# Kernel optimization log

Hardware: AMD Instinct MI355X
Metric: run time of the kernel (lower is better)

The kernel has to match this reference:

```python
import jax, jax.numpy as jnp
import numpy as np

NUM_EMBEDDINGS = 512
EMBEDDING_DIM = 64
COMMITMENT_COST = 0.25


def setup_inputs() -> dict:
    key = jax.random.key(0)
    k1, k2 = jax.random.split(key)
    x = jax.random.normal(k1, (32, 64, 64, 64), dtype=jnp.float32)  # [B, C=D, H, W]
    # torch init: uniform(-1/K, 1/K)
    w = jax.random.uniform(k2, (NUM_EMBEDDINGS, EMBEDDING_DIM), dtype=jnp.float32,
                           minval=-1.0 / NUM_EMBEDDINGS, maxval=1.0 / NUM_EMBEDDINGS)
    return {"x": x, "w": w}


def reference(x, w):
    # [B, C, H, W] -> [B, H, W, C]
    xt = jnp.transpose(x, (0, 2, 3, 1))
    flat = xt.reshape(-1, EMBEDDING_DIM)  # [N, D]
    # squared L2 distances to each codebook vector: [N, K]
    distances = (jnp.sum(flat * flat, axis=1, keepdims=True)
                 + jnp.sum(w * w, axis=1)
                 - 2.0 * flat @ w.T)
    idx = jnp.argmin(distances, axis=1)  # [N]
    encodings = jax.nn.one_hot(idx, NUM_EMBEDDINGS, dtype=x.dtype)  # [N, K]
    quantized = w[idx].reshape(xt.shape)  # gather == one_hot @ w
    e_latent_loss = jnp.mean((jax.lax.stop_gradient(quantized) - xt) ** 2)
    q_latent_loss = jnp.mean((quantized - jax.lax.stop_gradient(xt)) ** 2)
    quant_loss = q_latent_loss + COMMITMENT_COST * e_latent_loss
    # straight-through estimator
    quantized_st = xt + jax.lax.stop_gradient(quantized - xt)
    quantized_out = jnp.transpose(quantized_st, (0, 3, 1, 2))  # back to [B, C, H, W]
    avg_probs = jnp.mean(encodings, axis=0)
    perplexity = jnp.exp(-jnp.sum(avg_probs * jnp.log(avg_probs + 1e-10)))
    return quantized_out, quant_loss, encodings, perplexity
```

## Files before the change

### kernel.cpp

```cpp
#include <hip/hip_runtime.h>
#include <math.h>

#define TB        256
#define POSB      64
#define GROUPS    4
#define KPG       128
#define NPOS      131072
#define KCODES    512
#define DIM       64
#define HW        4096
#define LOSS_OFF  8388608ull
#define ENC_OFF   8388609ull
#define PERP_OFF  75497473ull

__device__ __forceinline__ float tree8(float r0, float r1, float r2, float r3,
                                       float r4, float r5, float r6, float r7) {
    return __fadd_rn(__fadd_rn(__fadd_rn(r0, r1), __fadd_rn(r2, r3)),
                     __fadd_rn(__fadd_rn(r4, r5), __fadd_rn(r6, r7)));
}

extern "C" __global__ __launch_bounds__(512)
void vq_prep(const float* __restrict__ w, float* __restrict__ ww,
             int* __restrict__ counts, float* __restrict__ lossAcc)
{
    const int k = threadIdx.x;
    const float* wk = w + k * DIM;
    float r[8];
    #pragma unroll
    for (int i = 0; i < 8; ++i) {
        #pragma unroll
        for (int j = 0; j < 8; ++j) {
            float v = wk[i * 8 + j];
            float pp = __fmul_rn(v, v);
            r[j] = (i == 0) ? pp : __fadd_rn(r[j], pp);
        }
    }
    ww[k] = tree8(r[0], r[1], r[2], r[3], r[4], r[5], r[6], r[7]);
    counts[k] = 0;
    if (k == 0) *lossAcc = 0.0f;
}

extern "C" __global__ __launch_bounds__(TB)
__attribute__((amdgpu_waves_per_eu(2, 4)))
void vq_main(const float* __restrict__ x, const float* __restrict__ w,
             const float* __restrict__ ww, float* __restrict__ out,
             int* __restrict__ counts, float* __restrict__ lossAcc)
{
    __shared__ float cdist[GROUPS][POSB];
    __shared__ int   ckidx[GROUPS][POSB];
    __shared__ int   hcount[KCODES];

    const int tid = threadIdx.x;
    const int l   = tid & 63;
    const int g   = __builtin_amdgcn_readfirstlane(tid >> 6);
    const int n   = blockIdx.x * POSB + l;
    const int b   = n >> 12;
    const int hw  = n & 4095;

    hcount[tid]      = 0;
    hcount[tid + TB] = 0;

    const float* xp = x + ((size_t)b * DIM) * HW + hw;
    float x2[DIM];
    float r[8];
    #pragma unroll
    for (int i = 0; i < 8; ++i) {
        #pragma unroll
        for (int j = 0; j < 8; ++j) {
            const int d = i * 8 + j;
            float v = xp[(size_t)d * HW];
            x2[d] = v + v;
            float pp = __fmul_rn(v, v);
            r[j] = (i == 0) ? pp : __fadd_rn(r[j], pp);
        }
    }
    const float A = tree8(r[0], r[1], r[2], r[3], r[4], r[5], r[6], r[7]);

    float best  = INFINITY;
    int   bestk = 0;
    const size_t T0 = ENC_OFF + (size_t)blockIdx.x * (POSB * KCODES);
    float4* zs4 = reinterpret_cast<float4*>(out + T0 + 3);
    const float4 zero4 = make_float4(0.0f, 0.0f, 0.0f, 0.0f);

    for (int kk = 0; kk < KPG; ++kk) {
        const int k = g * KPG + kk;
        const float* wk = w + (size_t)k * DIM;
        float s[8];
        #pragma unroll
        for (int i = 0; i < 8; ++i) {
            #pragma unroll
            for (int j = 0; j < 8; ++j) {
                const int d = i * 8 + j;
                if (i == 0) s[j] = __fmul_rn(x2[d], wk[d]);
                else        s[j] = __fmaf_rn(x2[d], wk[d], s[j]);
            }
        }
        float dot  = tree8(s[0], s[1], s[2], s[3], s[4], s[5], s[6], s[7]);
        float t    = __fadd_rn(A, ww[k]);
        float dist = __fadd_rn(t, -dot);
        if (dist < best) { best = dist; bestk = k; }

        if ((kk & 3) == 0) {
            const int m = (kk >> 2) * TB + tid;
            if (m < 8191) zs4[m] = zero4;
        }
    }
    cdist[g][l] = best;
    ckidx[g][l] = bestk;

    if (tid < 3)  out[T0 + tid]   = 0.0f;
    if (tid == 3) out[T0 + 32767] = 0.0f;

    __syncthreads();

    float fb = cdist[0][l];
    int   fk = ckidx[0][l];
    #pragma unroll
    for (int gg = 1; gg < GROUPS; ++gg) {
        float dg = cdist[gg][l];
        int   kg = ckidx[gg][l];
        if (dg < fb) { fb = dg; fk = kg; }
    }

    if (g == 0) {
        out[ENC_OFF + (size_t)n * KCODES + fk] = 1.0f;
        atomicAdd(&hcount[fk], 1);

        const float4* wrow = reinterpret_cast<const float4*>(w + (size_t)fk * DIM);
        float* qo = out + ((size_t)b * DIM) * HW + hw;
        float sse = 0.0f;
        #pragma unroll
        for (int c = 0; c < 16; ++c) {
            float4 q = wrow[c];
            qo[(size_t)(4 * c + 0) * HW] = q.x;
            qo[(size_t)(4 * c + 1) * HW] = q.y;
            qo[(size_t)(4 * c + 2) * HW] = q.z;
            qo[(size_t)(4 * c + 3) * HW] = q.w;
            float e0 = q.x - 0.5f * x2[4 * c + 0]; sse = __fmaf_rn(e0, e0, sse);
            float e1 = q.y - 0.5f * x2[4 * c + 1]; sse = __fmaf_rn(e1, e1, sse);
            float e2 = q.z - 0.5f * x2[4 * c + 2]; sse = __fmaf_rn(e2, e2, sse);
            float e3 = q.w - 0.5f * x2[4 * c + 3]; sse = __fmaf_rn(e3, e3, sse);
        }
        #pragma unroll
        for (int off = 32; off > 0; off >>= 1) sse += __shfl_down(sse, off);
        if (l == 0) atomicAdd(lossAcc, sse);
    }

    __syncthreads();

    {
        int c0 = hcount[tid];       if (c0) atomicAdd(&counts[tid], c0);
        int c1 = hcount[tid + TB];  if (c1) atomicAdd(&counts[tid + TB], c1);
    }
}

extern "C" __global__ __launch_bounds__(512)
void vq_finalize(const int* __restrict__ counts, const float* __restrict__ lossAcc,
                 float* __restrict__ out)
{
    __shared__ double sred[KCODES];
    const int t = threadIdx.x;
    double p = (double)counts[t] * (1.0 / (double)NPOS);
    sred[t] = -p * log(p + 1e-10);
    __syncthreads();
    for (int s = KCODES / 2; s > 0; s >>= 1) {
        if (t < s) sred[t] += sred[t + s];
        __syncthreads();
    }
    if (t == 0) {
        out[PERP_OFF] = (float)exp(sred[0]);
        out[LOSS_OFF] = 1.25f * (lossAcc[0] / 8388608.0f);
    }
}

extern "C" void kernel_launch(void* const* d_in, const int* in_sizes, int n_in,
                              void* d_out, int out_size, void* d_ws, size_t ws_size,
                              hipStream_t stream)
{
    const float* x = (const float*)d_in[0];
    const float* w = (const float*)d_in[1];
    float* out = (float*)d_out;

    float* ww      = (float*)d_ws;
    int*   counts  = (int*)((char*)d_ws + 2048);
    float* lossAcc = (float*)((char*)d_ws + 4096);

    vq_prep<<<1, 512, 0, stream>>>(w, ww, counts, lossAcc);
    vq_main<<<NPOS / POSB, TB, 0, stream>>>(x, w, ww, out, counts, lossAcc);
    vq_finalize<<<1, 512, 0, stream>>>(counts, lossAcc, out);
}
```

Measured before the change: 450.2 us.

## Split one-hot zero fill into separate kernel and raise scan occupancy

Moves zeroing of the 256 MB one-hot encodings buffer out of the distance-scan loop into a dedicated streaming fill kernel launched before the scan. The scan kernel gets a higher waves-per-EU hint (4-8) and stores the doubled input as float4 registers. Fill order versus the scan's one-hot writes stays correct because both kernels run in order on the same stream. The intent is to let the write-bound fill and the compute-bound scan each run at their own best occupancy. The cost is an extra launch, and the fill no longer hides behind the FMA work.

```diff
diff --git a/kernel.cpp b/kernel.cpp
--- a/kernel.cpp
+++ b/kernel.cpp
@@ -12,6 +12,7 @@
 #define LOSS_OFF  8388608ull
 #define ENC_OFF   8388609ull
 #define PERP_OFF  75497473ull
+#define ENC_LEN   67108864ull
 
 __device__ __forceinline__ float tree8(float r0, float r1, float r2, float r3,
                                        float r4, float r5, float r6, float r7) {
@@ -40,9 +41,27 @@
     if (k == 0) *lossAcc = 0.0f;
 }
 
+extern "C" __global__ __launch_bounds__(256)
+void vq_fill(float* __restrict__ out)
+{
+    const float4 zero4 = make_float4(0.0f, 0.0f, 0.0f, 0.0f);
+    float4* dst = reinterpret_cast<float4*>(out + ENC_OFF + 3);
+    const size_t base = (size_t)blockIdx.x * (256 * 8) + threadIdx.x;
+    #pragma unroll
+    for (int i = 0; i < 8; ++i) {
+        const size_t m = base + (size_t)i * 256;
+        if (m < 16777215ull) dst[m] = zero4;
+    }
+    if (blockIdx.x == 0 && threadIdx.x < 4) {
+        const size_t d = (threadIdx.x < 3) ? (ENC_OFF + threadIdx.x)
+                                           : (ENC_OFF + ENC_LEN - 1);
+        out[d] = 0.0f;
+    }
+}
+
 extern "C" __global__ __launch_bounds__(TB)
-__attribute__((amdgpu_waves_per_eu(2, 4)))
-void vq_main(const float* __restrict__ x, const float* __restrict__ w,
+__attribute__((amdgpu_waves_per_eu(4, 8)))
+void vq_scan(const float* __restrict__ x, const float* __restrict__ w,
              const float* __restrict__ ww, float* __restrict__ out,
              int* __restrict__ counts, float* __restrict__ lossAcc)
 {
@@ -61,55 +80,54 @@
     hcount[tid + TB] = 0;
 
     const float* xp = x + ((size_t)b * DIM) * HW + hw;
-    float x2[DIM];
+    float4 x2[16];
     float r[8];
     #pragma unroll
-    for (int i = 0; i < 8; ++i) {
-        #pragma unroll
-        for (int j = 0; j < 8; ++j) {
-            const int d = i * 8 + j;
-            float v = xp[(size_t)d * HW];
-            x2[d] = v + v;
-            float pp = __fmul_rn(v, v);
-            r[j] = (i == 0) ? pp : __fadd_rn(r[j], pp);
-        }
+    for (int c = 0; c < 16; ++c) {
+        float v0 = xp[(size_t)(4 * c + 0) * HW];
+        float v1 = xp[(size_t)(4 * c + 1) * HW];
+        float v2 = xp[(size_t)(4 * c + 2) * HW];
+        float v3 = xp[(size_t)(4 * c + 3) * HW];
+        x2[c].x = v0 + v0; x2[c].y = v1 + v1;
+        x2[c].z = v2 + v2; x2[c].w = v3 + v3;
+        const int j = (c & 1) * 4;
+        float p0 = __fmul_rn(v0, v0), p1 = __fmul_rn(v1, v1);
+        float p2 = __fmul_rn(v2, v2), p3 = __fmul_rn(v3, v3);
+        if (c < 2) { r[j] = p0; r[j+1] = p1; r[j+2] = p2; r[j+3] = p3; }
+        else { r[j]   = __fadd_rn(r[j],   p0); r[j+1] = __fadd_rn(r[j+1], p1);
+               r[j+2] = __fadd_rn(r[j+2], p2); r[j+3] = __fadd_rn(r[j+3], p3); }
     }
     const float A = tree8(r[0], r[1], r[2], r[3], r[4], r[5], r[6], r[7]);
 
     float best  = INFINITY;
     int   bestk = 0;
-    const size_t T0 = ENC_OFF + (size_t)blockIdx.x * (POSB * KCODES);
-    float4* zs4 = reinterpret_cast<float4*>(out + T0 + 3);
-    const float4 zero4 = make_float4(0.0f, 0.0f, 0.0f, 0.0f);
-
     for (int kk = 0; kk < KPG; ++kk) {
         const int k = g * KPG + kk;
         const float* wk = w + (size_t)k * DIM;
         float s[8];
         #pragma unroll
-        for (int i = 0; i < 8; ++i) {
-            #pragma unroll
-            for (int j = 0; j < 8; ++j) {
-                const int d = i * 8 + j;
-                if (i == 0) s[j] = __fmul_rn(x2[d], wk[d]);
-                else        s[j] = __fmaf_rn(x2[d], wk[d], s[j]);
+        for (int c = 0; c < 16; ++c) {
+            const int j = (c & 1) * 4;
+            const float* wc = wk + 4 * c;
+            if (c < 2) {
+                s[j]   = __fmul_rn(x2[c].x, wc[0]);
+                s[j+1] = __fmul_rn(x2[c].y, wc[1]);
+                s[j+2] = __fmul_rn(x2[c].z, wc[2]);
+                s[j+3] = __fmul_rn(x2[c].w, wc[3]);
+            } else {
+                s[j]   = __fmaf_rn(x2[c].x, wc[0], s[j]);
+                s[j+1] = __fmaf_rn(x2[c].y, wc[1], s[j+1]);
+                s[j+2] = __fmaf_rn(x2[c].z, wc[2], s[j+2]);
+                s[j+3] = __fmaf_rn(x2[c].w, wc[3], s[j+3]);
             }
         }
         float dot  = tree8(s[0], s[1], s[2], s[3], s[4], s[5], s[6], s[7]);
         float t    = __fadd_rn(A, ww[k]);
         float dist = __fadd_rn(t, -dot);
         if (dist < best) { best = dist; bestk = k; }
-
-        if ((kk & 3) == 0) {
-            const int m = (kk >> 2) * TB + tid;
-            if (m < 8191) zs4[m] = zero4;
-        }
     }
     cdist[g][l] = best;
     ckidx[g][l] = bestk;
-
-    if (tid < 3)  out[T0 + tid]   = 0.0f;
-    if (tid == 3) out[T0 + 32767] = 0.0f;
 
     __syncthreads();
 
@@ -136,10 +154,10 @@
             qo[(size_t)(4 * c + 1) * HW] = q.y;
             qo[(size_t)(4 * c + 2) * HW] = q.z;
             qo[(size_t)(4 * c + 3) * HW] = q.w;
-            float e0 = q.x - 0.5f * x2[4 * c + 0]; sse = __fmaf_rn(e0, e0, sse);
-            float e1 = q.y - 0.5f * x2[4 * c + 1]; sse = __fmaf_rn(e1, e1, sse);
-            float e2 = q.z - 0.5f * x2[4 * c + 2]; sse = __fmaf_rn(e2, e2, sse);
-            float e3 = q.w - 0.5f * x2[4 * c + 3]; sse = __fmaf_rn(e3, e3, sse);
+            float e0 = q.x - 0.5f * x2[c].x; sse = __fmaf_rn(e0, e0, sse);
+            float e1 = q.y - 0.5f * x2[c].y; sse = __fmaf_rn(e1, e1, sse);
+            float e2 = q.z - 0.5f * x2[c].z; sse = __fmaf_rn(e2, e2, sse);
+            float e3 = q.w - 0.5f * x2[c].w; sse = __fmaf_rn(e3, e3, sse);
         }
         #pragma unroll
         for (int off = 32; off > 0; off >>= 1) sse += __shfl_down(sse, off);
@@ -186,6 +204,7 @@
     float* lossAcc = (float*)((char*)d_ws + 4096);
 
     vq_prep<<<1, 512, 0, stream>>>(w, ww, counts, lossAcc);
-    vq_main<<<NPOS / POSB, TB, 0, stream>>>(x, w, ww, out, counts, lossAcc);
+    vq_fill<<<8192, 256, 0, stream>>>(out);
+    vq_scan<<<NPOS / POSB, TB, 0, stream>>>(x, w, ww, out, counts, lossAcc);
     vq_finalize<<<1, 512, 0, stream>>>(counts, lossAcc, out);
 }
```

New measurement: 523.5 us. +16.3%, slower.

## Stage x rows in LDS, cooperatively load, and process two codes per iteration

Applied to the files above, without the earlier changes.

Each of the four waves now loads a quarter of the 64 channels for the block's positions into a padded LDS array, so x is read from global memory once per block instead of once per wave. The distance loop reads x from LDS and evaluates two codebook rows per iteration, giving two independent FMA chains and sharing each LDS load between them. The waves_per_eu hint is removed, and the encoding-zeroing stores are reissued on the new two-code schedule. In exchange, every FMA now needs an LDS read where it used a register before, which may limit the inner loop, and the added LDS use may lower occupancy.

```diff
diff --git a/kernel.cpp b/kernel.cpp
--- a/kernel.cpp
+++ b/kernel.cpp
@@ -5,10 +5,12 @@
 #define POSB      64
 #define GROUPS    4
 #define KPG       128
+#define KB        2
 #define NPOS      131072
 #define KCODES    512
 #define DIM       64
 #define HW        4096
+#define STRIDE    65
 #define LOSS_OFF  8388608ull
 #define ENC_OFF   8388609ull
 #define PERP_OFF  75497473ull
@@ -41,11 +43,11 @@
 }
 
 extern "C" __global__ __launch_bounds__(TB)
-__attribute__((amdgpu_waves_per_eu(2, 4)))
-void vq_main(const float* __restrict__ x, const float* __restrict__ w,
+void vq_scan(const float* __restrict__ x, const float* __restrict__ w,
              const float* __restrict__ ww, float* __restrict__ out,
              int* __restrict__ counts, float* __restrict__ lossAcc)
 {
+    __shared__ float x2ls[POSB * STRIDE];
     __shared__ float cdist[GROUPS][POSB];
     __shared__ int   ckidx[GROUPS][POSB];
     __shared__ int   hcount[KCODES];
@@ -61,16 +63,22 @@
     hcount[tid + TB] = 0;
 
     const float* xp = x + ((size_t)b * DIM) * HW + hw;
-    float x2[DIM];
+    float* row = &x2ls[l * STRIDE];
+    #pragma unroll
+    for (int t = 0; t < 16; ++t) {
+        const int d = 16 * g + t;
+        float v = xp[(size_t)d * HW];
+        row[d] = v + v;
+    }
+    __syncthreads();
+
     float r[8];
     #pragma unroll
     for (int i = 0; i < 8; ++i) {
         #pragma unroll
         for (int j = 0; j < 8; ++j) {
-            const int d = i * 8 + j;
-            float v = xp[(size_t)d * HW];
-            x2[d] = v + v;
-            float pp = __fmul_rn(v, v);
+            float xe = 0.5f * row[i * 8 + j];
+            float pp = __fmul_rn(xe, xe);
             r[j] = (i == 0) ? pp : __fadd_rn(r[j], pp);
         }
     }
@@ -82,26 +90,40 @@
     float4* zs4 = reinterpret_cast<float4*>(out + T0 + 3);
     const float4 zero4 = make_float4(0.0f, 0.0f, 0.0f, 0.0f);
 
-    for (int kk = 0; kk < KPG; ++kk) {
-        const int k = g * KPG + kk;
-        const float* wk = w + (size_t)k * DIM;
-        float s[8];
-        #pragma unroll
-        for (int i = 0; i < 8; ++i) {
-            #pragma unroll
-            for (int j = 0; j < 8; ++j) {
-                const int d = i * 8 + j;
-                if (i == 0) s[j] = __fmul_rn(x2[d], wk[d]);
-                else        s[j] = __fmaf_rn(x2[d], wk[d], s[j]);
+    for (int p = 0; p < KPG / KB; ++p) {
+        const int k0 = g * KPG + p * KB;
+        const float* w0 = w + (size_t)k0 * DIM;
+        float s0[8], s1[8];
+        #pragma unroll
+        for (int c = 0; c < 16; ++c) {
+            const int j = (c & 1) * 4;
+            float xa = row[4 * c + 0];
+            float xb = row[4 * c + 1];
+            float xc = row[4 * c + 2];
+            float xd = row[4 * c + 3];
+            const float* wc0 = w0 + 4 * c;
+            const float* wc1 = w0 + DIM + 4 * c;
+            if (c < 2) {
+                s0[j]   = __fmul_rn(xa, wc0[0]);  s1[j]   = __fmul_rn(xa, wc1[0]);
+                s0[j+1] = __fmul_rn(xb, wc0[1]);  s1[j+1] = __fmul_rn(xb, wc1[1]);
+                s0[j+2] = __fmul_rn(xc, wc0[2]);  s1[j+2] = __fmul_rn(xc, wc1[2]);
+                s0[j+3] = __fmul_rn(xd, wc0[3]);  s1[j+3] = __fmul_rn(xd, wc1[3]);
+            } else {
+                s0[j]   = __fmaf_rn(xa, wc0[0], s0[j]);    s1[j]   = __fmaf_rn(xa, wc1[0], s1[j]);
+                s0[j+1] = __fmaf_rn(xb, wc0[1], s0[j+1]);  s1[j+1] = __fmaf_rn(xb, wc1[1], s1[j+1]);
+                s0[j+2] = __fmaf_rn(xc, wc0[2], s0[j+2]);  s1[j+2] = __fmaf_rn(xc, wc1[2], s1[j+2]);
+                s0[j+3] = __fmaf_rn(xd, wc0[3], s0[j+3]);  s1[j+3] = __fmaf_rn(xd, wc1[3], s1[j+3]);
             }
         }
-        float dot  = tree8(s[0], s[1], s[2], s[3], s[4], s[5], s[6], s[7]);
-        float t    = __fadd_rn(A, ww[k]);
-        float dist = __fadd_rn(t, -dot);
-        if (dist < best) { best = dist; bestk = k; }
-
-        if ((kk & 3) == 0) {
-            const int m = (kk >> 2) * TB + tid;
+        float dot0  = tree8(s0[0], s0[1], s0[2], s0[3], s0[4], s0[5], s0[6], s0[7]);
+        float dot1  = tree8(s1[0], s1[1], s1[2], s1[3], s1[4], s1[5], s1[6], s1[7]);
+        float dist0 = __fadd_rn(__fadd_rn(A, ww[k0]),     -dot0);
+        float dist1 = __fadd_rn(__fadd_rn(A, ww[k0 + 1]), -dot1);
+        if (dist0 < best) { best = dist0; bestk = k0; }
+        if (dist1 < best) { best = dist1; bestk = k0 + 1; }
+
+        if (p < 32) {
+            const int m = p * TB + tid;
             if (m < 8191) zs4[m] = zero4;
         }
     }
@@ -136,10 +158,10 @@
             qo[(size_t)(4 * c + 1) * HW] = q.y;
             qo[(size_t)(4 * c + 2) * HW] = q.z;
             qo[(size_t)(4 * c + 3) * HW] = q.w;
-            float e0 = q.x - 0.5f * x2[4 * c + 0]; sse = __fmaf_rn(e0, e0, sse);
-            float e1 = q.y - 0.5f * x2[4 * c + 1]; sse = __fmaf_rn(e1, e1, sse);
-            float e2 = q.z - 0.5f * x2[4 * c + 2]; sse = __fmaf_rn(e2, e2, sse);
-            float e3 = q.w - 0.5f * x2[4 * c + 3]; sse = __fmaf_rn(e3, e3, sse);
+            float e0 = q.x - 0.5f * row[4 * c + 0]; sse = __fmaf_rn(e0, e0, sse);
+            float e1 = q.y - 0.5f * row[4 * c + 1]; sse = __fmaf_rn(e1, e1, sse);
+            float e2 = q.z - 0.5f * row[4 * c + 2]; sse = __fmaf_rn(e2, e2, sse);
+            float e3 = q.w - 0.5f * row[4 * c + 3]; sse = __fmaf_rn(e3, e3, sse);
         }
         #pragma unroll
         for (int off = 32; off > 0; off >>= 1) sse += __shfl_down(sse, off);
@@ -186,6 +208,6 @@
     float* lossAcc = (float*)((char*)d_ws + 4096);
 
     vq_prep<<<1, 512, 0, stream>>>(w, ww, counts, lossAcc);
-    vq_main<<<NPOS / POSB, TB, 0, stream>>>(x, w, ww, out, counts, lossAcc);
+    vq_scan<<<NPOS / POSB, TB, 0, stream>>>(x, w, ww, out, counts, lossAcc);
     vq_finalize<<<1, 512, 0, stream>>>(counts, lossAcc, out);
 }
```

Result: slower. 526.9 us (+17.1%).
